# Kernel optimization log

Hardware: AMD Instinct MI355X
Metric: run time of the kernel (lower is better)

The kernel has to match this reference:

```python
import jax, jax.numpy as jnp
import numpy as np

K_HEADS = 8
D_HEAD = 64
D = K_HEADS * D_HEAD  # 512
B, TP, TQ, N = 8, 48, 48, 256


def setup_inputs() -> dict:
    key = jax.random.key(0)
    ks = jax.random.split(key, 13)
    s = 1.0 / np.sqrt(D)
    inp = {
        "X": jax.random.normal(ks[0], (B, TP, N, D), jnp.float32),
        "STE_P": jax.random.normal(ks[1], (B, TP, N, D), jnp.float32),
        "STE_Q": jax.random.normal(ks[2], (B, TQ, N, D), jnp.float32),
        "Wq": jax.random.uniform(ks[3], (D, D), jnp.float32, -s, s),
        "bq": jax.random.uniform(ks[4], (D,), jnp.float32, -s, s),
        "Wk": jax.random.uniform(ks[5], (D, D), jnp.float32, -s, s),
        "bk": jax.random.uniform(ks[6], (D,), jnp.float32, -s, s),
        "Wv": jax.random.uniform(ks[7], (D, D), jnp.float32, -s, s),
        "bv": jax.random.uniform(ks[8], (D,), jnp.float32, -s, s),
        "W1": jax.random.uniform(ks[9], (D, D), jnp.float32, -s, s),
        "b1": jax.random.uniform(ks[10], (D,), jnp.float32, -s, s),
        "W2": jax.random.uniform(ks[11], (D, D), jnp.float32, -s, s),
        "b2": jax.random.uniform(ks[12], (D,), jnp.float32, -s, s),
    }
    return inp


def reference(X, STE_P, STE_Q, Wq, bq, Wk, bk, Wv, bv, W1, b1, W2, b2):
    # ReLU-fused QKV projections
    q = jax.nn.relu(STE_Q @ Wq + bq)  # [B, Tq, N, D]
    k = jax.nn.relu(STE_P @ Wk + bk)  # [B, Tp, N, D]
    v = jax.nn.relu(X @ Wv + bv)      # [B, Tp, N, D]

    # split(last, d) + cat(dim 0) == introduce head axis h of size K
    b, tq, n, _ = q.shape
    tp = k.shape[1]
    q = q.reshape(b, tq, n, K_HEADS, D_HEAD)
    k = k.reshape(b, tp, n, K_HEADS, D_HEAD)
    v = v.reshape(b, tp, n, K_HEADS, D_HEAD)

    # attention over the TIME axis, per node and head: scores [b,h,n,tq,tp]
    scale = 1.0 / jnp.sqrt(jnp.asarray(D_HEAD, q.dtype))
    attn = jnp.einsum('bqnhd,bpnhd->bhnqp', q, k) * scale
    attn = jax.nn.softmax(attn, axis=-1)
    out = jnp.einsum('bhnqp,bpnhd->bqnhd', attn, v).reshape(b, tq, n, D)

    out = jax.nn.relu(out @ W1 + b1) @ W2 + b2
    return out
```

## Files before the change

kernel.cpp:

```cpp
#include <hip/hip_runtime.h>

typedef _Float16 f16;
typedef __fp16 hf2 __attribute__((ext_vector_type(2)));
typedef _Float16 f16x4 __attribute__((ext_vector_type(4)));
typedef _Float16 f16x8 __attribute__((ext_vector_type(8)));
typedef float f32x4 __attribute__((ext_vector_type(4)));

typedef const __attribute__((address_space(1))) unsigned int guint;
typedef __attribute__((address_space(3))) unsigned int luint;
__device__ __forceinline__ void gl_lds16(const void* g, void* l) {
    __builtin_amdgcn_global_load_lds((guint*)g, (luint*)l, 16, 0, 0);
}

__global__ __launch_bounds__(256) void wconv(const float* w0, const float* w1, const float* w2,
                                             const float* w3, const float* w4, f16* dst) {
    const float* src;
    switch (blockIdx.z) { case 0: src = w0; break; case 1: src = w1; break;
                          case 2: src = w2; break; case 3: src = w3; break; default: src = w4; }
    __shared__ float tile[32][33];
    int k0 = blockIdx.x * 32, n0 = blockIdx.y * 32;
    int t = threadIdx.x;
    int r = t >> 3, c4 = (t & 7) * 4;
    float4 v = *(const float4*)(src + (k0 + r) * 512 + n0 + c4);
    tile[r][c4 + 0] = v.x; tile[r][c4 + 1] = v.y; tile[r][c4 + 2] = v.z; tile[r][c4 + 3] = v.w;
    __syncthreads();
    f16x4 o;
    o[0] = (f16)tile[c4 + 0][r]; o[1] = (f16)tile[c4 + 1][r];
    o[2] = (f16)tile[c4 + 2][r]; o[3] = (f16)tile[c4 + 3][r];
    *(f16x4*)(dst + (size_t)blockIdx.z * 262144 + (n0 + r) * 512 + k0 + c4) = o;
}

template <bool A16, bool RELU, bool O16>
__global__ __launch_bounds__(512) void gemm_w8(const void* __restrict__ Ap,
                                               const f16* __restrict__ Bt,
                                               const float* __restrict__ bias,
                                               void* __restrict__ Cp) {
    constexpr int ASZ = A16 ? 16384 : 32768;
    constexpr int BSZ = 8192;
    constexpr int BUF = ASZ + BSZ;
    __shared__ __align__(16) char smem[2 * BUF];

    const int cpx = gridDim.x >> 3;
    const int orig = blockIdx.x;
    const int wgid = (orig & 7) * cpx + (orig >> 3);
    const int by = wgid & 3;
    const int bx = wgid >> 2;
    const int r0 = bx * 256, c0 = by * 128;

    const int t = threadIdx.x;
    const int j = t & 63, w = t >> 6;
    const int lr = j & 15, lq = j >> 4;
    const int wr = (w >> 1) * 64, wc = (w & 1) * 64;

    const char* aSrc;
    if (A16) aSrc = (const char*)Ap + ((size_t)(r0 + (t >> 2)) * 512 + ((t & 3) ^ ((t >> 3) & 3)) * 8) * 2;
    else     aSrc = (const char*)Ap + ((size_t)(r0 + (t >> 3)) * 512 + ((t & 7) ^ ((t >> 3) & 7)) * 4) * 4;
    const char* bSrc = (const char*)Bt + ((size_t)(c0 + (t >> 2)) * 512 + ((t & 3) ^ ((t >> 3) & 3)) * 8) * 2;

    int aoffL[4], aoffH[4], boff[4];
#pragma unroll
    for (int m = 0; m < 4; m++) {
        int row = wr + m * 16 + lr;
        if (A16) {
            aoffL[m] = row * 64 + ((lq ^ ((row >> 1) & 3)) << 4);
        } else {
            int s = row & 7;
            aoffL[m] = row * 128 + (((2 * lq) ^ s) << 4);
            aoffH[m] = row * 128 + (((2 * lq + 1) ^ s) << 4);
        }
    }
#pragma unroll
    for (int nb = 0; nb < 4; nb++) {
        int row = wc + nb * 16 + lr;
        boff[nb] = ASZ + row * 64 + ((lq ^ ((row >> 1) & 3)) << 4);
    }

    f32x4 acc[4][4] = {};

#define STAGE(tk, buf)                                                     \
    do {                                                                   \
        char* al_ = smem + (buf) * BUF + t * 16;                           \
        if (A16) {                                                         \
            const char* as_ = aSrc + (size_t)(tk) * 64;                    \
            gl_lds16(as_, al_);                                            \
            gl_lds16(as_ + 131072, al_ + 8192);                            \
        } else {                                                           \
            const char* as_ = aSrc + (size_t)(tk) * 128;                   \
            gl_lds16(as_, al_);                                            \
            gl_lds16(as_ + 131072, al_ + 8192);                            \
            gl_lds16(as_ + 262144, al_ + 16384);                           \
            gl_lds16(as_ + 393216, al_ + 24576);                           \
        }                                                                  \
        const char* bs_ = bSrc + (size_t)(tk) * 64;                        \
        gl_lds16(bs_, smem + (buf) * BUF + ASZ + t * 16);                  \
    } while (0)

#define COMPUTE(buf)                                                       \
    do {                                                                   \
        const char* sb_ = smem + (buf) * BUF;                              \
        f16x8 av[4], bv[4];                                                \
        _Pragma("unroll")                                                  \
        for (int m = 0; m < 4; m++) {                                      \
            if (A16) {                                                     \
                av[m] = *(const f16x8*)(sb_ + aoffL[m]);                   \
            } else {                                                       \
                float4 x0 = *(const float4*)(sb_ + aoffL[m]);              \
                float4 x1 = *(const float4*)(sb_ + aoffH[m]);              \
                hf2 p0 = __builtin_amdgcn_cvt_pkrtz(x0.x, x0.y);           \
                hf2 p1 = __builtin_amdgcn_cvt_pkrtz(x0.z, x0.w);           \
                hf2 p2 = __builtin_amdgcn_cvt_pkrtz(x1.x, x1.y);           \
                hf2 p3 = __builtin_amdgcn_cvt_pkrtz(x1.z, x1.w);           \
                f16x8 h;                                                   \
                h[0] = (f16)p0[0]; h[1] = (f16)p0[1]; h[2] = (f16)p1[0]; h[3] = (f16)p1[1]; \
                h[4] = (f16)p2[0]; h[5] = (f16)p2[1]; h[6] = (f16)p3[0]; h[7] = (f16)p3[1]; \
                av[m] = h;                                                 \
            }                                                              \
        }                                                                  \
        _Pragma("unroll")                                                  \
        for (int nb = 0; nb < 4; nb++) bv[nb] = *(const f16x8*)(sb_ + boff[nb]); \
        _Pragma("unroll")                                                  \
        for (int m = 0; m < 4; m++)                                        \
            _Pragma("unroll")                                              \
            for (int nb = 0; nb < 4; nb++)                                 \
                acc[m][nb] = __builtin_amdgcn_mfma_f32_16x16x32_f16(av[m], bv[nb], acc[m][nb], 0, 0, 0); \
    } while (0)

    STAGE(0, 0);
    __syncthreads();
    int cur = 0;
#pragma unroll 1
    for (int tk = 0; tk < 16; ++tk) {
        if (tk < 15) STAGE(tk + 1, cur ^ 1);
        COMPUTE(cur);
        __syncthreads();
        cur ^= 1;
    }
#undef STAGE
#undef COMPUTE

#pragma unroll
    for (int nb = 0; nb < 4; nb++) {
        int col = c0 + wc + nb * 16 + lr;
        float b = bias[col];
#pragma unroll
        for (int m = 0; m < 4; m++) {
#pragma unroll
            for (int r = 0; r < 4; r++) {
                float v = acc[m][nb][r] + b;
                if (RELU) v = fmaxf(v, 0.0f);
                size_t row = (size_t)(r0 + wr + m * 16 + lq * 4 + r);
                if (O16) ((f16*)Cp)[row * 512 + col] = (f16)v;
                else     ((float*)Cp)[row * 512 + col] = v;
            }
        }
    }
}

__global__ __launch_bounds__(64) void attn_kernel(const f16* __restrict__ q,
                                                  const f16* __restrict__ k,
                                                  const f16* __restrict__ v,
                                                  f16* __restrict__ out) {
    const int h = blockIdx.x, n = blockIdx.y, b = blockIdx.z;
    __shared__ f16 sQ[48 * 72];
    __shared__ f16 sK[48 * 72];
    __shared__ f16 sP[48 * 72];
    __shared__ f16 sVt[64 * 72];
    const int l = threadIdx.x, lr = l & 15, lq = l >> 4;
    const size_t rowstride = 256 * 512;
    const size_t base = ((size_t)(b * 48) * 256 + n) * 512 + h * 64;

    const int pr = l >> 3, pc = (l & 7) * 8;
#pragma unroll
    for (int pass = 0; pass < 6; pass++) {
        int row = pass * 8 + pr;
        size_t g = base + (size_t)row * rowstride + pc;
        f16x8 qv = *(const f16x8*)(q + g);
        f16x8 kv = *(const f16x8*)(k + g);
        f16x8 vv = *(const f16x8*)(v + g);
        *(f16x8*)&sQ[row * 72 + pc] = qv;
        *(f16x8*)&sK[row * 72 + pc] = kv;
#pragma unroll
        for (int j = 0; j < 8; j++) sVt[(pc + j) * 72 + row] = vv[j];
    }
    {
        f16x8 z = {};
        *(f16x8*)&sVt[l * 72 + 48] = z;
        *(f16x8*)&sVt[l * 72 + 56] = z;
        if (l < 48) { *(f16x8*)&sP[l * 72 + 48] = z; *(f16x8*)&sP[l * 72 + 56] = z; }
    }
    __syncthreads();

    f32x4 s[3][3] = {};
#pragma unroll
    for (int ks = 0; ks < 2; ks++) {
        f16x8 aq[3], bk[3];
#pragma unroll
        for (int m = 0; m < 3; m++)  aq[m] = *(const f16x8*)&sQ[(m * 16 + lr) * 72 + ks * 32 + lq * 8];
#pragma unroll
        for (int nb = 0; nb < 3; nb++) bk[nb] = *(const f16x8*)&sK[(nb * 16 + lr) * 72 + ks * 32 + lq * 8];
#pragma unroll
        for (int m = 0; m < 3; m++)
#pragma unroll
            for (int nb = 0; nb < 3; nb++)
                s[m][nb] = __builtin_amdgcn_mfma_f32_16x16x32_f16(aq[m], bk[nb], s[m][nb], 0, 0, 0);
    }

#pragma unroll
    for (int m = 0; m < 3; m++) {
#pragma unroll
        for (int r = 0; r < 4; r++) {
            float a0 = s[m][0][r] * 0.125f, a1 = s[m][1][r] * 0.125f, a2 = s[m][2][r] * 0.125f;
            float mx = fmaxf(a0, fmaxf(a1, a2));
#pragma unroll
            for (int d = 1; d < 16; d <<= 1) mx = fmaxf(mx, __shfl_xor(mx, d));
            float e0 = __expf(a0 - mx), e1 = __expf(a1 - mx), e2 = __expf(a2 - mx);
            float sm = e0 + e1 + e2;
#pragma unroll
            for (int d = 1; d < 16; d <<= 1) sm += __shfl_xor(sm, d);
            float inv = 1.0f / sm;
            int row = m * 16 + lq * 4 + r;
            sP[row * 72 + 0  + lr] = (f16)(e0 * inv);
            sP[row * 72 + 16 + lr] = (f16)(e1 * inv);
            sP[row * 72 + 32 + lr] = (f16)(e2 * inv);
        }
    }
    __syncthreads();

    f32x4 o[3][4] = {};
#pragma unroll
    for (int ks = 0; ks < 2; ks++) {
        f16x8 ap[3], bvv[4];
#pragma unroll
        for (int m = 0; m < 3; m++)  ap[m] = *(const f16x8*)&sP[(m * 16 + lr) * 72 + ks * 32 + lq * 8];
#pragma unroll
        for (int nb = 0; nb < 4; nb++) bvv[nb] = *(const f16x8*)&sVt[(nb * 16 + lr) * 72 + ks * 32 + lq * 8];
#pragma unroll
        for (int m = 0; m < 3; m++)
#pragma unroll
            for (int nb = 0; nb < 4; nb++)
                o[m][nb] = __builtin_amdgcn_mfma_f32_16x16x32_f16(ap[m], bvv[nb], o[m][nb], 0, 0, 0);
    }

#pragma unroll
    for (int m = 0; m < 3; m++)
#pragma unroll
        for (int nb = 0; nb < 4; nb++)
#pragma unroll
            for (int r = 0; r < 4; r++) {
                int row = m * 16 + lq * 4 + r;
                out[base + (size_t)row * rowstride + nb * 16 + lr] = (f16)o[m][nb][r];
            }
}

extern "C" void kernel_launch(void* const* d_in, const int* in_sizes, int n_in,
                              void* d_out, int out_size, void* d_ws, size_t ws_size,
                              hipStream_t stream) {
    const float* X    = (const float*)d_in[0];
    const float* STEP = (const float*)d_in[1];
    const float* STEQ = (const float*)d_in[2];
    const float* Wq   = (const float*)d_in[3];
    const float* bq   = (const float*)d_in[4];
    const float* Wk   = (const float*)d_in[5];
    const float* bk   = (const float*)d_in[6];
    const float* Wv   = (const float*)d_in[7];
    const float* bv   = (const float*)d_in[8];
    const float* W1   = (const float*)d_in[9];
    const float* b1   = (const float*)d_in[10];
    const float* W2   = (const float*)d_in[11];
    const float* b2   = (const float*)d_in[12];
    float* out = (float*)d_out;

    const size_t MROWS = 98304;
    f16* ws  = (f16*)d_ws;
    f16* Wqt = ws;
    f16* Wkt = ws + 262144;
    f16* Wvt = ws + 524288;
    f16* W1t = ws + 786432;
    f16* W2t = ws + 1048576;
    f16* qb  = ws + 1310720;
    f16* kb  = qb + MROWS * 512;
    f16* vb  = kb + MROWS * 512;
    f16* attn = qb;
    f16* hb   = kb;

    wconv<<<dim3(16, 16, 5), 256, 0, stream>>>(Wq, Wk, Wv, W1, W2, ws);

    gemm_w8<false, true, true><<<1536, 512, 0, stream>>>(STEQ, Wqt, bq, qb);
    gemm_w8<false, true, true><<<1536, 512, 0, stream>>>(STEP, Wkt, bk, kb);
    gemm_w8<false, true, true><<<1536, 512, 0, stream>>>(X,    Wvt, bv, vb);

    attn_kernel<<<dim3(8, 256, 8), 64, 0, stream>>>(qb, kb, vb, attn);

    gemm_w8<true, true,  true ><<<1536, 512, 0, stream>>>(attn, W1t, b1, hb);
    gemm_w8<true, false, false><<<1536, 512, 0, stream>>>(hb,   W2t, b2, out);
}
```

Baseline: 628.4 us.

## Add 256x256 four-stage pipelined GEMM for the W1/W2 projections

Adds a new f16 GEMM kernel with 256x256 output tiles, a 4-deep LDS ring buffer fed by direct global-to-LDS loads, explicit vmcnt waits, raw barriers and XOR-swizzled LDS layout. It also remaps workgroups across 8 groups (XCD-aware ordering) and uses setprio around the MFMA blocks. It replaces the older gemm_w8 only for the two output-side GEMMs, halving the grid, to raise data reuse and overlap loads with MFMA work. Larger tiles use more registers and 128KB LDS per block, which may limit occupancy.

```diff
diff --git a/kernel.cpp b/kernel.cpp
--- a/kernel.cpp
+++ b/kernel.cpp
@@ -11,6 +11,13 @@
 __device__ __forceinline__ void gl_lds16(const void* g, void* l) {
     __builtin_amdgcn_global_load_lds((guint*)g, (luint*)l, 16, 0, 0);
 }
+template <int N>
+__device__ __forceinline__ void vmwait() {
+    if constexpr (N == 8)       asm volatile("s_waitcnt vmcnt(8)" ::: "memory");
+    else if constexpr (N == 4)  asm volatile("s_waitcnt vmcnt(4)" ::: "memory");
+    else                        asm volatile("s_waitcnt vmcnt(0)" ::: "memory");
+}
+__device__ __forceinline__ void barrier_raw() { __builtin_amdgcn_s_barrier(); __builtin_amdgcn_sched_barrier(0); }
 
 __global__ __launch_bounds__(256) void wconv(const float* w0, const float* w1, const float* w2,
                                              const float* w3, const float* w4, f16* dst) {
@@ -156,6 +163,113 @@
     }
 }
 
+template <bool RELU, bool O16>
+__global__ __launch_bounds__(512, 2) void gemm_8ph(const f16* __restrict__ A,
+                                                   const f16* __restrict__ Bt,
+                                                   const float* __restrict__ bias,
+                                                   void* __restrict__ Cp) {
+    constexpr int BUFSZ = 32768;
+    __shared__ __align__(16) char smem[4 * BUFSZ];
+
+    const int cpx = gridDim.x >> 3;
+    const int orig = blockIdx.x;
+    const int wgid = (orig & 7) * cpx + (orig >> 3);
+    const int by = wgid & 1;
+    const int bx = wgid >> 1;
+    const int r0 = bx * 256, c0 = by * 256;
+
+    const int t = threadIdx.x;
+    const int j = t & 63, w = t >> 6;
+    const int lr = j & 15, lq = j >> 4;
+    const int wr = (w >> 2) * 128, wc = (w & 3) * 64;
+
+    const int srow = t >> 2;
+    const int sblk = (t & 3) ^ ((t >> 3) & 3);
+    const f16* aS = A  + (size_t)(r0 + srow) * 512 + sblk * 8;
+    const f16* bS = Bt + (size_t)(c0 + srow) * 512 + sblk * 8;
+    const int dstT = t * 16;
+
+    int aoff[8], boff[4];
+#pragma unroll
+    for (int m = 0; m < 8; m++) {
+        int row = wr + m * 16 + lr;
+        aoff[m] = row * 64 + ((lq ^ ((row >> 1) & 3)) << 4);
+    }
+#pragma unroll
+    for (int nb = 0; nb < 4; nb++) {
+        int row = wc + nb * 16 + lr;
+        boff[nb] = 16384 + row * 64 + ((lq ^ ((row >> 1) & 3)) << 4);
+    }
+
+    f32x4 acc[8][4] = {};
+
+    auto stageA = [&](int kt) {
+        char* d = smem + (kt & 3) * BUFSZ + dstT;
+        const f16* s = aS + kt * 32;
+        gl_lds16(s, d);
+        gl_lds16(s + 65536, d + 8192);
+    };
+    auto stageB = [&](int kt) {
+        char* d = smem + (kt & 3) * BUFSZ + 16384 + dstT;
+        const f16* s = bS + kt * 32;
+        gl_lds16(s, d);
+        gl_lds16(s + 65536, d + 8192);
+    };
+
+    stageA(0); stageB(0); stageA(1); stageB(1); stageA(2); stageB(2);
+
+#pragma unroll 1
+    for (int kt = 0; kt < 16; ++kt) {
+        const char* sb = smem + (kt & 3) * BUFSZ;
+        if (kt <= 13)      vmwait<8>();
+        else if (kt == 14) vmwait<4>();
+        else               vmwait<0>();
+        barrier_raw();
+        if (kt < 13) stageA(kt + 3);
+        f16x8 bfr[4], afr[4];
+#pragma unroll
+        for (int nb = 0; nb < 4; nb++) bfr[nb] = *(const f16x8*)(sb + boff[nb]);
+#pragma unroll
+        for (int m = 0; m < 4; m++) afr[m] = *(const f16x8*)(sb + aoff[m]);
+        __builtin_amdgcn_s_setprio(1);
+#pragma unroll
+        for (int m = 0; m < 4; m++)
+#pragma unroll
+            for (int nb = 0; nb < 4; nb++)
+                acc[m][nb] = __builtin_amdgcn_mfma_f32_16x16x32_f16(afr[m], bfr[nb], acc[m][nb], 0, 0, 0);
+        __builtin_amdgcn_s_setprio(0);
+        barrier_raw();
+        if (kt < 13) stageB(kt + 3);
+        f16x8 afr2[4];
+#pragma unroll
+        for (int m = 0; m < 4; m++) afr2[m] = *(const f16x8*)(sb + aoff[m + 4]);
+        __builtin_amdgcn_s_setprio(1);
+#pragma unroll
+        for (int m = 0; m < 4; m++)
+#pragma unroll
+            for (int nb = 0; nb < 4; nb++)
+                acc[m + 4][nb] = __builtin_amdgcn_mfma_f32_16x16x32_f16(afr2[m], bfr[nb], acc[m + 4][nb], 0, 0, 0);
+        __builtin_amdgcn_s_setprio(0);
+    }
+
+#pragma unroll
+    for (int nb = 0; nb < 4; nb++) {
+        int col = c0 + wc + nb * 16 + lr;
+        float b = bias[col];
+#pragma unroll
+        for (int m = 0; m < 8; m++) {
+#pragma unroll
+            for (int r = 0; r < 4; r++) {
+                float v = acc[m][nb][r] + b;
+                if (RELU) v = fmaxf(v, 0.0f);
+                size_t row = (size_t)(r0 + wr + m * 16 + lq * 4 + r);
+                if (O16) ((f16*)Cp)[row * 512 + col] = (f16)v;
+                else     ((float*)Cp)[row * 512 + col] = v;
+            }
+        }
+    }
+}
+
 __global__ __launch_bounds__(64) void attn_kernel(const f16* __restrict__ q,
                                                   const f16* __restrict__ k,
                                                   const f16* __restrict__ v,
@@ -180,7 +294,7 @@
         *(f16x8*)&sQ[row * 72 + pc] = qv;
         *(f16x8*)&sK[row * 72 + pc] = kv;
 #pragma unroll
-        for (int j = 0; j < 8; j++) sVt[(pc + j) * 72 + row] = vv[j];
+        for (int jj = 0; jj < 8; jj++) sVt[(pc + jj) * 72 + row] = vv[jj];
     }
     {
         f16x8 z = {};
@@ -291,6 +405,6 @@
 
     attn_kernel<<<dim3(8, 256, 8), 64, 0, stream>>>(qb, kb, vb, attn);
 
-    gemm_w8<true, true,  true ><<<1536, 512, 0, stream>>>(attn, W1t, b1, hb);
-    gemm_w8<true, false, false><<<1536, 512, 0, stream>>>(hb,   W2t, b2, out);
-}
+    gemm_8ph<true,  true ><<<768, 512, 0, stream>>>(attn, W1t, b1, hb);
+    gemm_8ph<false, false><<<768, 512, 0, stream>>>(hb,   W2t, b2, out);
+}
```

Measured after the change: 620.3 us. No clear change (-1.3%).
